# Performance work log

Measured on AMD Instinct MI355X. Metric: run time of the kernel, lower is better.

The kernel has to match this reference:

```python
import jax, jax.numpy as jnp
import numpy as np

EMBED_DIM = 768
NUM_HEADS = 12
HEAD_DIM = EMBED_DIM // NUM_HEADS
SCALE = HEAD_DIM ** -0.5
B, N = 8, 1024


def setup_inputs() -> dict:
    key = jax.random.key(0)
    ks = jax.random.split(key, 5)
    return {
        "x": jax.random.normal(ks[0], (B, N, EMBED_DIM), dtype=jnp.float32),
        "qkv_w": jax.random.normal(ks[1], (3 * EMBED_DIM, EMBED_DIM), dtype=jnp.float32) * 0.02,
        "qkv_b": jax.random.normal(ks[2], (3 * EMBED_DIM,), dtype=jnp.float32) * 0.02,
        "proj_w": jax.random.normal(ks[3], (EMBED_DIM, EMBED_DIM), dtype=jnp.float32) * 0.02,
        "proj_b": jax.random.normal(ks[4], (EMBED_DIM,), dtype=jnp.float32) * 0.02,
    }


def reference(x, qkv_w, qkv_b, proj_w, proj_b):
    b, n, c = x.shape
    h, hd = NUM_HEADS, HEAD_DIM
    # QKV projection: [b,n,3c]
    qkv = jnp.einsum("bnc,dc->bnd", x, qkv_w) + qkv_b
    qkv = qkv.reshape(b, n, 3, h, hd).transpose(2, 0, 3, 1, 4)  # [3,b,h,n,hd]
    q, k, v = qkv[0], qkv[1], qkv[2]
    # scaled dot-product attention (eager path; dropout is identity in eval)
    attn = jnp.einsum("bhqd,bhkd->bhqk", q, k) * SCALE
    attn = jax.nn.softmax(attn, axis=-1)
    out = jnp.einsum("bhqk,bhkd->bhqd", attn, v)  # [b,h,n,hd]
    out = out.transpose(0, 2, 1, 3).reshape(b, n, c)
    # output projection
    return jnp.einsum("bnc,dc->bnd", out, proj_w) + proj_b
```

## Files before the change

kernel.cpp:

```cpp
#include <hip/hip_runtime.h>
#include <hip/hip_bf16.h>

typedef __attribute__((ext_vector_type(4))) float f32x4;
typedef __attribute__((ext_vector_type(8))) short short8;
typedef unsigned short u16;

#define MFMA(a, b, c) __builtin_amdgcn_mfma_f32_16x16x32_bf16((a), (b), (c), 0, 0, 0)

#define WAITVM_BAR(N) do {                                          \
    asm volatile("s_waitcnt vmcnt(" #N ")" ::: "memory");           \
    __builtin_amdgcn_s_barrier();                                   \
    __builtin_amdgcn_sched_barrier(0);                              \
} while (0)
#define BAR2() do {                                                 \
    __builtin_amdgcn_sched_barrier(0);                              \
    __builtin_amdgcn_s_barrier();                                   \
    __builtin_amdgcn_sched_barrier(0);                              \
} while (0)

static constexpr int EMBED = 768;
static constexpr int NH = 12;
static constexpr int HD = 64;
static constexpr int BATCH = 8;
static constexpr int SEQ = 1024;

__device__ __forceinline__ u16 f2bu(float f) {
    __hip_bfloat16 h = __float2bfloat16(f);
    u16 u; __builtin_memcpy(&u, &h, 2); return u;
}
__device__ __forceinline__ float exp2a(float x) {
    float r; asm("v_exp_f32 %0, %1" : "=v"(r) : "v"(x)); return r;
}
__device__ __forceinline__ unsigned cvt_pk_bf16(float lo, float hi) {
    unsigned r; asm("v_cvt_pk_bf16_f32 %0, %1, %2" : "=v"(r) : "v"(lo), "v"(hi)); return r;
}
__device__ __forceinline__ float max3f(float a, float b, float c) {
    return fmaxf(fmaxf(a, b), c);
}

__global__ void cvt_bf16_k(const float* __restrict__ in, u16* __restrict__ out, int n) {
    int i = (blockIdx.x * blockDim.x + threadIdx.x) * 4;
    if (i >= n) return;
    float4 v = *reinterpret_cast<const float4*>(in + i);
    ushort4 o;
    o.x = f2bu(v.x); o.y = f2bu(v.y); o.z = f2bu(v.z); o.w = f2bu(v.w);
    *reinterpret_cast<ushort4*>(out + i) = o;
}

template <int EPI>
__global__ __launch_bounds__(256)
void gemm_bt_k(const u16* __restrict__ A, const u16* __restrict__ Bw,
               const float* __restrict__ bias,
               u16* __restrict__ q_out, u16* __restrict__ k_out,
               u16* __restrict__ vt_out, float* __restrict__ f_out)
{
    __shared__ __attribute__((aligned(16))) char smem[65536];
    const int tid  = threadIdx.x;
    const int wave = tid >> 6, lane = tid & 63;
    const int hi   = lane >> 4, l15 = lane & 15;
    const int wr   = wave >> 1, wc = wave & 1;
    const int bm   = blockIdx.x, bn = blockIdx.y;

    f32x4 acc[4][4] = {};

    const size_t arow0 = (size_t)bm * 128;
    const size_t brow0 = (size_t)bn * 128;

    auto stage = [&](int buf, int kt) {
        char* Ab = smem + buf * 32768;
        char* Bb = Ab + 16384;
#pragma unroll
        for (int c = 0; c < 4; ++c) {
            int ck   = c * 4 + wave;
            int p    = ck * 1024 + lane * 16;
            int row  = p >> 7;
            int pcol = (p & 127) ^ ((row & 7) << 4);
            const u16* srcA = A  + (arow0 + row) * EMBED + kt + (pcol >> 1);
            const u16* srcB = Bw + (brow0 + row) * EMBED + kt + (pcol >> 1);
            __builtin_amdgcn_global_load_lds((const __attribute__((address_space(1))) void*)srcA,
                                             (__attribute__((address_space(3))) void*)(Ab + ck * 1024), 16, 0, 0);
            __builtin_amdgcn_global_load_lds((const __attribute__((address_space(1))) void*)srcB,
                                             (__attribute__((address_space(3))) void*)(Bb + ck * 1024), 16, 0, 0);
        }
    };

    auto comp = [&](const char* Ab, const char* Bb) {
#pragma unroll
        for (int kk = 0; kk < 2; ++kk) {
            short8 af[4], bf[4];
#pragma unroll
            for (int mi = 0; mi < 4; ++mi) {
                int R  = wr * 64 + mi * 16 + l15;
                int Cb = kk * 64 + hi * 16;
                af[mi] = *reinterpret_cast<const short8*>(Ab + R * 128 + (Cb ^ ((R & 7) << 4)));
            }
#pragma unroll
            for (int ni = 0; ni < 4; ++ni) {
                int R  = wc * 64 + ni * 16 + l15;
                int Cb = kk * 64 + hi * 16;
                bf[ni] = *reinterpret_cast<const short8*>(Bb + R * 128 + (Cb ^ ((R & 7) << 4)));
            }
#pragma unroll
            for (int mi = 0; mi < 4; ++mi)
#pragma unroll
                for (int ni = 0; ni < 4; ++ni)
                    acc[mi][ni] = MFMA(af[mi], bf[ni], acc[mi][ni]);
        }
    };

    const char* A0 = smem;
    const char* B0 = smem + 16384;
    const char* A1 = smem + 32768;
    const char* B1 = smem + 49152;

    stage(0, 0);
#pragma unroll
    for (int tt = 0; tt < 5; ++tt) {
        stage(1, (2 * tt + 1) * 64);
        WAITVM_BAR(8);
        comp(A0, B0);
        BAR2();
        stage(0, (2 * tt + 2) * 64);
        WAITVM_BAR(8);
        comp(A1, B1);
        BAR2();
    }
    stage(1, 11 * 64);
    WAITVM_BAR(8);
    comp(A0, B0);
    BAR2();
    WAITVM_BAR(0);
    comp(A1, B1);

#pragma unroll
    for (int mi = 0; mi < 4; ++mi) {
        int crow0 = bm * 128 + wr * 64 + mi * 16 + hi * 4;
#pragma unroll
        for (int ni = 0; ni < 4; ++ni) {
            int ccol = bn * 128 + wc * 64 + ni * 16 + l15;
            float bv = bias[ccol];
            if constexpr (EPI == 0) {
                int which = ccol / 768;
                int rem   = ccol - which * 768;
                int hh = rem >> 6, hd = rem & 63;
                int bb = crow0 >> 10, nn0 = crow0 & 1023;
                size_t bh = (size_t)(bb * NH + hh);
                if (which == 2) {
                    uint2 pk;
                    pk.x = cvt_pk_bf16(acc[mi][ni][0] + bv, acc[mi][ni][1] + bv);
                    pk.y = cvt_pk_bf16(acc[mi][ni][2] + bv, acc[mi][ni][3] + bv);
                    *reinterpret_cast<uint2*>(&vt_out[(bh * HD + hd) * SEQ + nn0]) = pk;
                } else if (which == 0) {
#pragma unroll
                    for (int r = 0; r < 4; ++r)
                        q_out[(bh * SEQ + nn0 + r) * HD + hd] =
                            f2bu((acc[mi][ni][r] + bv) * 0.18033688f);
                } else {
#pragma unroll
                    for (int r = 0; r < 4; ++r)
                        k_out[(bh * SEQ + nn0 + r) * HD + hd] = f2bu(acc[mi][ni][r] + bv);
                }
            } else {
#pragma unroll
                for (int r = 0; r < 4; ++r)
                    f_out[(size_t)(crow0 + r) * EMBED + ccol] = acc[mi][ni][r] + bv;
            }
        }
    }
}

__global__ __launch_bounds__(256)
void attn_k(const u16* __restrict__ Q, const u16* __restrict__ K,
            const u16* __restrict__ Vt, u16* __restrict__ AO)
{
    __shared__ __attribute__((aligned(16))) u16 kls[2][4096];
    __shared__ __attribute__((aligned(16))) u16 vls[2][4096];
    __shared__ __attribute__((aligned(16))) u16 plds[4][32][72];

    const int tid = threadIdx.x;
    const int w   = tid >> 6, lane = tid & 63;
    const int hi  = lane >> 4, l15 = lane & 15;
    const int f   = blockIdx.x;
    const int xcd = f & 7, i = f >> 3;
    const int bh  = xcd * 12 + (i % 12);
    const int q0w = (i / 12) * 128 + w * 32;

    const u16* Qh = Q  + (size_t)bh * SEQ * HD;
    const u16* Kh = K  + (size_t)bh * SEQ * HD;
    const u16* Vh = Vt + (size_t)bh * HD * SEQ;

    auto stage = [&](int buf, int kt) {
#pragma unroll
        for (int c = 0; c < 4; ++c) {
            int ch   = c * 4 + w;
            int mc   = ch & 7;
            int p    = mc * 1024 + lane * 16;
            int row  = p >> 7;
            int colb = (p & 127) ^ ((row & 7) << 4);
            const u16* src;
            u16* dst;
            if (ch < 8) { src = Kh + (size_t)(kt + row) * HD + (colb >> 1); dst = kls[buf] + mc * 512; }
            else        { src = Vh + (size_t)row * SEQ + kt + (colb >> 1);  dst = vls[buf] + mc * 512; }
            __builtin_amdgcn_global_load_lds((const __attribute__((address_space(1))) void*)src,
                                             (__attribute__((address_space(3))) void*)dst, 16, 0, 0);
        }
    };

    stage(0, 0);

    short8 qf[2][2];
#pragma unroll
    for (int qh = 0; qh < 2; ++qh)
#pragma unroll
        for (int dh = 0; dh < 2; ++dh)
            qf[qh][dh] = *reinterpret_cast<const short8*>(
                Qh + (size_t)(q0w + qh * 16 + l15) * HD + dh * 32 + hi * 8);

    f32x4 accO[4][2] = {};
    float m0 = -1e30f, m1 = -1e30f, lp0 = 0.f, lp1 = 0.f;

    auto tile = [&](const u16* Kb, const u16* Vb) {
        f32x4 st[4][2] = {};
#pragma unroll
        for (int kb = 0; kb < 4; ++kb) {
            int R  = kb * 16 + l15;
            int sw = (R & 7) << 4;
            short8 kf0 = *reinterpret_cast<const short8*>(Kb + R * 64 + (((hi * 16) ^ sw) >> 1));
            short8 kf1 = *reinterpret_cast<const short8*>(Kb + R * 64 + (((64 + hi * 16) ^ sw) >> 1));
            st[kb][0] = MFMA(kf0, qf[0][0], st[kb][0]);
            st[kb][0] = MFMA(kf1, qf[0][1], st[kb][0]);
            st[kb][1] = MFMA(kf0, qf[1][0], st[kb][1]);
            st[kb][1] = MFMA(kf1, qf[1][1], st[kb][1]);
        }

        float p0 = max3f(st[0][0][0], st[0][0][1], st[0][0][2]);
        float p1 = max3f(st[0][0][3], st[1][0][0], st[1][0][1]);
        float p2 = max3f(st[1][0][2], st[1][0][3], st[2][0][0]);
        float p3 = max3f(st[2][0][1], st[2][0][2], st[2][0][3]);
        float p4 = max3f(st[3][0][0], st[3][0][1], st[3][0][2]);
        float tm0 = max3f(max3f(p0, p1, p2), max3f(p3, p4, st[3][0][3]), -1e30f);
        float r0 = max3f(st[0][1][0], st[0][1][1], st[0][1][2]);
        float r1 = max3f(st[0][1][3], st[1][1][0], st[1][1][1]);
        float r2 = max3f(st[1][1][2], st[1][1][3], st[2][1][0]);
        float r3 = max3f(st[2][1][1], st[2][1][2], st[2][1][3]);
        float r4 = max3f(st[3][1][0], st[3][1][1], st[3][1][2]);
        float tm1 = max3f(max3f(r0, r1, r2), max3f(r3, r4, st[3][1][3]), -1e30f);
        tm0 = fmaxf(tm0, __shfl_xor(tm0, 16, 64));
        tm0 = fmaxf(tm0, __shfl_xor(tm0, 32, 64));
        tm1 = fmaxf(tm1, __shfl_xor(tm1, 16, 64));
        tm1 = fmaxf(tm1, __shfl_xor(tm1, 32, 64));
        if (!__all((tm0 <= m0 + 8.f) && (tm1 <= m1 + 8.f))) {
            float mn0 = fmaxf(m0, tm0), mn1 = fmaxf(m1, tm1);
            float sc0 = exp2a(m0 - mn0), sc1 = exp2a(m1 - mn1);
            m0 = mn0; m1 = mn1;
            lp0 *= sc0; lp1 *= sc1;
#pragma unroll
            for (int db = 0; db < 4; ++db)
#pragma unroll
                for (int r = 0; r < 4; ++r) {
                    accO[db][0][r] *= sc0;
                    accO[db][1][r] *= sc1;
                }
        }

#pragma unroll
        for (int kb = 0; kb < 4; ++kb) {
            float e0 = exp2a(st[kb][0][0] - m0);
            float e1 = exp2a(st[kb][0][1] - m0);
            float e2 = exp2a(st[kb][0][2] - m0);
            float e3 = exp2a(st[kb][0][3] - m0);
            lp0 += (e0 + e1) + (e2 + e3);
            unsigned* d0 = reinterpret_cast<unsigned*>(&plds[w][l15][kb * 16 + hi * 4]);
            d0[0] = cvt_pk_bf16(e0, e1);
            d0[1] = cvt_pk_bf16(e2, e3);
            float g0 = exp2a(st[kb][1][0] - m1);
            float g1 = exp2a(st[kb][1][1] - m1);
            float g2 = exp2a(st[kb][1][2] - m1);
            float g3 = exp2a(st[kb][1][3] - m1);
            lp1 += (g0 + g1) + (g2 + g3);
            unsigned* d1 = reinterpret_cast<unsigned*>(&plds[w][16 + l15][kb * 16 + hi * 4]);
            d1[0] = cvt_pk_bf16(g0, g1);
            d1[1] = cvt_pk_bf16(g2, g3);
        }

        short8 pa[2][2];
#pragma unroll
        for (int qh = 0; qh < 2; ++qh)
#pragma unroll
            for (int kk = 0; kk < 2; ++kk)
                pa[qh][kk] = *reinterpret_cast<const short8*>(&plds[w][qh * 16 + l15][kk * 32 + hi * 8]);
        __builtin_amdgcn_sched_barrier(0);

#pragma unroll
        for (int db = 0; db < 4; ++db) {
            int R  = db * 16 + l15;
            int sw = (R & 7) << 4;
            short8 vf0 = *reinterpret_cast<const short8*>(Vb + R * 64 + (((hi * 16) ^ sw) >> 1));
            short8 vf1 = *reinterpret_cast<const short8*>(Vb + R * 64 + (((64 + hi * 16) ^ sw) >> 1));
            accO[db][0] = MFMA(vf0, pa[0][0], accO[db][0]);
            accO[db][0] = MFMA(vf1, pa[0][1], accO[db][0]);
            accO[db][1] = MFMA(vf0, pa[1][0], accO[db][1]);
            accO[db][1] = MFMA(vf1, pa[1][1], accO[db][1]);
        }
    };

    for (int tt = 0; tt < 7; ++tt) {
        stage(1, (2 * tt + 1) * 64);
        WAITVM_BAR(4);
        tile(kls[0], vls[0]);
        BAR2();
        stage(0, (2 * tt + 2) * 64);
        WAITVM_BAR(4);
        tile(kls[1], vls[1]);
        BAR2();
    }
    stage(1, 15 * 64);
    WAITVM_BAR(4);
    tile(kls[0], vls[0]);
    BAR2();
    WAITVM_BAR(0);
    tile(kls[1], vls[1]);

    lp0 += __shfl_xor(lp0, 16, 64);
    lp0 += __shfl_xor(lp0, 32, 64);
    lp1 += __shfl_xor(lp1, 16, 64);
    lp1 += __shfl_xor(lp1, 32, 64);
    float linv0 = 1.f / lp0, linv1 = 1.f / lp1;
    const int bb = bh / NH, hh = bh - bb * NH;
#pragma unroll
    for (int qh = 0; qh < 2; ++qh) {
        float linv = qh ? linv1 : linv0;
        size_t rowb = ((size_t)bb * SEQ + q0w + qh * 16 + l15) * EMBED + hh * HD;
#pragma unroll
        for (int db = 0; db < 4; ++db) {
            float o0 = accO[db][qh][0] * linv, o1 = accO[db][qh][1] * linv;
            float o2 = accO[db][qh][2] * linv, o3 = accO[db][qh][3] * linv;
            uint2 pkd;
            pkd.x = cvt_pk_bf16(o0, o1);
            pkd.y = cvt_pk_bf16(o2, o3);
            *reinterpret_cast<uint2*>(&AO[rowb + db * 16 + hi * 4]) = pkd;
        }
    }
}

extern "C" void kernel_launch(void* const* d_in, const int* in_sizes, int n_in,
                              void* d_out, int out_size, void* d_ws, size_t ws_size,
                              hipStream_t stream)
{
    const float* x      = (const float*)d_in[0];
    const float* qkv_w  = (const float*)d_in[1];
    const float* qkv_b  = (const float*)d_in[2];
    const float* proj_w = (const float*)d_in[3];
    const float* proj_b = (const float*)d_in[4];
    float* out = (float*)d_out;

    char* ws = (char*)d_ws;
    u16* xb  = (u16*)(ws);
    u16* wb  = (u16*)(ws + 12582912);
    u16* pw  = (u16*)(ws + 16121856);
    u16* qb  = (u16*)(ws + 17301504);
    u16* kb  = (u16*)(ws + 29884416);
    u16* vt  = (u16*)(ws + 42467328);
    u16* ao  = (u16*)(ws + 55050240);

    cvt_bf16_k<<<6144, 256, 0, stream>>>(x,      xb, BATCH * SEQ * EMBED);
    cvt_bf16_k<<<1728, 256, 0, stream>>>(qkv_w,  wb, 3 * EMBED * EMBED);
    cvt_bf16_k<<<576,  256, 0, stream>>>(proj_w, pw, EMBED * EMBED);

    gemm_bt_k<0><<<dim3(64, 18), 256, 0, stream>>>(xb, wb, qkv_b, qb, kb, vt, nullptr);
    attn_k<<<768, 256, 0, stream>>>(qb, kb, vt, ao);
    gemm_bt_k<1><<<dim3(64, 6), 256, 0, stream>>>(ao, pw, proj_b, nullptr, nullptr, nullptr, out);
}
```

Baseline: 114.0 us.

## Use 8 waves of 16 query rows in attention and permute P in registers

The attention kernel now runs 512 threads per block, with each wave owning 16 query rows instead of 32. This halves per-wave registers and raises occupancy, and each wave now stages one K chunk and one V chunk. The P matrix is no longer round-tripped through LDS; it is rearranged into MFMA operand layout with v_permlane32/16_swap, which removes that LDS store, load and scratch buffer. s_setprio is set around the MFMA sections. In exchange, K and V fragments are reread from LDS by twice as many waves, and the lane permutation must match the MFMA layout exactly.

New measurement: 107.1 us. 6.1% less time.

```diff
diff --git a/kernel.cpp b/kernel.cpp
--- a/kernel.cpp
+++ b/kernel.cpp
@@ -36,6 +36,17 @@
 }
 __device__ __forceinline__ float max3f(float a, float b, float c) {
     return fmaxf(fmaxf(a, b), c);
+}
+__device__ __forceinline__ void swap32(unsigned& a, unsigned& b) {
+    asm volatile("v_permlane32_swap_b32 %0, %1" : "+v"(a), "+v"(b));
+}
+__device__ __forceinline__ void swap16(unsigned& a, unsigned& b) {
+    asm volatile("v_permlane16_swap_b32 %0, %1" : "+v"(a), "+v"(b));
+}
+__device__ __forceinline__ short8 mk8(unsigned w0, unsigned w1, unsigned w2, unsigned w3) {
+    union { unsigned u[4]; short8 s; } c;
+    c.u[0] = w0; c.u[1] = w1; c.u[2] = w2; c.u[3] = w3;
+    return c.s;
 }
 
 __global__ void cvt_bf16_k(const float* __restrict__ in, u16* __restrict__ out, int n) {
@@ -169,13 +180,12 @@
     }
 }
 
-__global__ __launch_bounds__(256)
+__global__ __launch_bounds__(512, 6)
 void attn_k(const u16* __restrict__ Q, const u16* __restrict__ K,
             const u16* __restrict__ Vt, u16* __restrict__ AO)
 {
     __shared__ __attribute__((aligned(16))) u16 kls[2][4096];
     __shared__ __attribute__((aligned(16))) u16 vls[2][4096];
-    __shared__ __attribute__((aligned(16))) u16 plds[4][32][72];
 
     const int tid = threadIdx.x;
     const int w   = tid >> 6, lane = tid & 63;
@@ -183,163 +193,137 @@
     const int f   = blockIdx.x;
     const int xcd = f & 7, i = f >> 3;
     const int bh  = xcd * 12 + (i % 12);
-    const int q0w = (i / 12) * 128 + w * 32;
+    const int q0w = (i / 12) * 128 + w * 16;
 
     const u16* Qh = Q  + (size_t)bh * SEQ * HD;
     const u16* Kh = K  + (size_t)bh * SEQ * HD;
     const u16* Vh = Vt + (size_t)bh * HD * SEQ;
 
-    auto stage = [&](int buf, int kt) {
-#pragma unroll
-        for (int c = 0; c < 4; ++c) {
-            int ch   = c * 4 + w;
-            int mc   = ch & 7;
-            int p    = mc * 1024 + lane * 16;
-            int row  = p >> 7;
-            int colb = (p & 127) ^ ((row & 7) << 4);
-            const u16* src;
-            u16* dst;
-            if (ch < 8) { src = Kh + (size_t)(kt + row) * HD + (colb >> 1); dst = kls[buf] + mc * 512; }
-            else        { src = Vh + (size_t)row * SEQ + kt + (colb >> 1);  dst = vls[buf] + mc * 512; }
-            __builtin_amdgcn_global_load_lds((const __attribute__((address_space(1))) void*)src,
-                                             (__attribute__((address_space(3))) void*)dst, 16, 0, 0);
-        }
+    const int sp    = w * 1024 + lane * 16;
+    const int srow  = sp >> 7;
+    const int scolb = (sp & 127) ^ ((srow & 7) << 4);
+    const u16* kbase = Kh + (size_t)srow * HD + (scolb >> 1);
+    const u16* vbase = Vh + (size_t)srow * SEQ + (scolb >> 1);
+
+    auto stage = [&](int buf, int t) {
+        __builtin_amdgcn_global_load_lds(
+            (const __attribute__((address_space(1))) void*)(kbase + (size_t)t * 64 * HD),
+            (__attribute__((address_space(3))) void*)(&kls[buf][w * 512]), 16, 0, 0);
+        __builtin_amdgcn_global_load_lds(
+            (const __attribute__((address_space(1))) void*)(vbase + (size_t)t * 64),
+            (__attribute__((address_space(3))) void*)(&vls[buf][w * 512]), 16, 0, 0);
     };
 
     stage(0, 0);
 
-    short8 qf[2][2];
-#pragma unroll
-    for (int qh = 0; qh < 2; ++qh)
-#pragma unroll
-        for (int dh = 0; dh < 2; ++dh)
-            qf[qh][dh] = *reinterpret_cast<const short8*>(
-                Qh + (size_t)(q0w + qh * 16 + l15) * HD + dh * 32 + hi * 8);
-
-    f32x4 accO[4][2] = {};
-    float m0 = -1e30f, m1 = -1e30f, lp0 = 0.f, lp1 = 0.f;
+    short8 qf[2];
+#pragma unroll
+    for (int dh = 0; dh < 2; ++dh)
+        qf[dh] = *reinterpret_cast<const short8*>(
+            Qh + (size_t)(q0w + l15) * HD + dh * 32 + hi * 8);
+
+    f32x4 accO[4] = {};
+    float m = -1e30f, lp = 0.f;
 
     auto tile = [&](const u16* Kb, const u16* Vb) {
-        f32x4 st[4][2] = {};
+        f32x4 st[4] = {};
+        __builtin_amdgcn_s_setprio(1);
 #pragma unroll
         for (int kb = 0; kb < 4; ++kb) {
             int R  = kb * 16 + l15;
             int sw = (R & 7) << 4;
             short8 kf0 = *reinterpret_cast<const short8*>(Kb + R * 64 + (((hi * 16) ^ sw) >> 1));
             short8 kf1 = *reinterpret_cast<const short8*>(Kb + R * 64 + (((64 + hi * 16) ^ sw) >> 1));
-            st[kb][0] = MFMA(kf0, qf[0][0], st[kb][0]);
-            st[kb][0] = MFMA(kf1, qf[0][1], st[kb][0]);
-            st[kb][1] = MFMA(kf0, qf[1][0], st[kb][1]);
-            st[kb][1] = MFMA(kf1, qf[1][1], st[kb][1]);
-        }
-
-        float p0 = max3f(st[0][0][0], st[0][0][1], st[0][0][2]);
-        float p1 = max3f(st[0][0][3], st[1][0][0], st[1][0][1]);
-        float p2 = max3f(st[1][0][2], st[1][0][3], st[2][0][0]);
-        float p3 = max3f(st[2][0][1], st[2][0][2], st[2][0][3]);
-        float p4 = max3f(st[3][0][0], st[3][0][1], st[3][0][2]);
-        float tm0 = max3f(max3f(p0, p1, p2), max3f(p3, p4, st[3][0][3]), -1e30f);
-        float r0 = max3f(st[0][1][0], st[0][1][1], st[0][1][2]);
-        float r1 = max3f(st[0][1][3], st[1][1][0], st[1][1][1]);
-        float r2 = max3f(st[1][1][2], st[1][1][3], st[2][1][0]);
-        float r3 = max3f(st[2][1][1], st[2][1][2], st[2][1][3]);
-        float r4 = max3f(st[3][1][0], st[3][1][1], st[3][1][2]);
-        float tm1 = max3f(max3f(r0, r1, r2), max3f(r3, r4, st[3][1][3]), -1e30f);
-        tm0 = fmaxf(tm0, __shfl_xor(tm0, 16, 64));
-        tm0 = fmaxf(tm0, __shfl_xor(tm0, 32, 64));
-        tm1 = fmaxf(tm1, __shfl_xor(tm1, 16, 64));
-        tm1 = fmaxf(tm1, __shfl_xor(tm1, 32, 64));
-        if (!__all((tm0 <= m0 + 8.f) && (tm1 <= m1 + 8.f))) {
-            float mn0 = fmaxf(m0, tm0), mn1 = fmaxf(m1, tm1);
-            float sc0 = exp2a(m0 - mn0), sc1 = exp2a(m1 - mn1);
-            m0 = mn0; m1 = mn1;
-            lp0 *= sc0; lp1 *= sc1;
+            st[kb] = MFMA(kf0, qf[0], st[kb]);
+            st[kb] = MFMA(kf1, qf[1], st[kb]);
+        }
+        __builtin_amdgcn_s_setprio(0);
+
+        float t0 = max3f(st[0][0], st[0][1], st[0][2]);
+        float t1 = max3f(st[0][3], st[1][0], st[1][1]);
+        float t2 = max3f(st[1][2], st[1][3], st[2][0]);
+        float t3 = max3f(st[2][1], st[2][2], st[2][3]);
+        float t4 = max3f(st[3][0], st[3][1], st[3][2]);
+        float tm = fmaxf(max3f(t0, t1, t2), max3f(t3, t4, st[3][3]));
+        tm = fmaxf(tm, __shfl_xor(tm, 16, 64));
+        tm = fmaxf(tm, __shfl_xor(tm, 32, 64));
+        if (!__all(tm <= m + 8.f)) {
+            float mn = fmaxf(m, tm);
+            float sc = exp2a(m - mn);
+            m = mn;
+            lp *= sc;
 #pragma unroll
             for (int db = 0; db < 4; ++db)
 #pragma unroll
-                for (int r = 0; r < 4; ++r) {
-                    accO[db][0][r] *= sc0;
-                    accO[db][1][r] *= sc1;
-                }
-        }
-
+                for (int r = 0; r < 4; ++r) accO[db][r] *= sc;
+        }
+
+        unsigned X[4][2];
 #pragma unroll
         for (int kb = 0; kb < 4; ++kb) {
-            float e0 = exp2a(st[kb][0][0] - m0);
-            float e1 = exp2a(st[kb][0][1] - m0);
-            float e2 = exp2a(st[kb][0][2] - m0);
-            float e3 = exp2a(st[kb][0][3] - m0);
-            lp0 += (e0 + e1) + (e2 + e3);
-            unsigned* d0 = reinterpret_cast<unsigned*>(&plds[w][l15][kb * 16 + hi * 4]);
-            d0[0] = cvt_pk_bf16(e0, e1);
-            d0[1] = cvt_pk_bf16(e2, e3);
-            float g0 = exp2a(st[kb][1][0] - m1);
-            float g1 = exp2a(st[kb][1][1] - m1);
-            float g2 = exp2a(st[kb][1][2] - m1);
-            float g3 = exp2a(st[kb][1][3] - m1);
-            lp1 += (g0 + g1) + (g2 + g3);
-            unsigned* d1 = reinterpret_cast<unsigned*>(&plds[w][16 + l15][kb * 16 + hi * 4]);
-            d1[0] = cvt_pk_bf16(g0, g1);
-            d1[1] = cvt_pk_bf16(g2, g3);
-        }
-
-        short8 pa[2][2];
-#pragma unroll
-        for (int qh = 0; qh < 2; ++qh)
-#pragma unroll
-            for (int kk = 0; kk < 2; ++kk)
-                pa[qh][kk] = *reinterpret_cast<const short8*>(&plds[w][qh * 16 + l15][kk * 32 + hi * 8]);
-        __builtin_amdgcn_sched_barrier(0);
-
+            float e0 = exp2a(st[kb][0] - m);
+            float e1 = exp2a(st[kb][1] - m);
+            float e2 = exp2a(st[kb][2] - m);
+            float e3 = exp2a(st[kb][3] - m);
+            lp += (e0 + e1) + (e2 + e3);
+            X[kb][0] = cvt_pk_bf16(e0, e1);
+            X[kb][1] = cvt_pk_bf16(e2, e3);
+        }
+
+        unsigned a0 = X[0][0], b0 = X[1][0];
+        swap32(a0, b0); swap16(a0, b0);
+        unsigned a1 = X[0][1], b1 = X[1][1];
+        swap32(a1, b1); swap16(a1, b1);
+        unsigned a2 = X[2][0], b2 = X[3][0];
+        swap32(a2, b2); swap16(a2, b2);
+        unsigned a3 = X[2][1], b3 = X[3][1];
+        swap32(a3, b3); swap16(a3, b3);
+        short8 pa0 = mk8(a0, a1, b0, b1);
+        short8 pa1 = mk8(a2, a3, b2, b3);
+
+        __builtin_amdgcn_s_setprio(1);
 #pragma unroll
         for (int db = 0; db < 4; ++db) {
             int R  = db * 16 + l15;
             int sw = (R & 7) << 4;
             short8 vf0 = *reinterpret_cast<const short8*>(Vb + R * 64 + (((hi * 16) ^ sw) >> 1));
             short8 vf1 = *reinterpret_cast<const short8*>(Vb + R * 64 + (((64 + hi * 16) ^ sw) >> 1));
-            accO[db][0] = MFMA(vf0, pa[0][0], accO[db][0]);
-            accO[db][0] = MFMA(vf1, pa[0][1], accO[db][0]);
-            accO[db][1] = MFMA(vf0, pa[1][0], accO[db][1]);
-            accO[db][1] = MFMA(vf1, pa[1][1], accO[db][1]);
-        }
+            accO[db] = MFMA(vf0, pa0, accO[db]);
+            accO[db] = MFMA(vf1, pa1, accO[db]);
+        }
+        __builtin_amdgcn_s_setprio(0);
     };
 
     for (int tt = 0; tt < 7; ++tt) {
-        stage(1, (2 * tt + 1) * 64);
-        WAITVM_BAR(4);
+        stage(1, 2 * tt + 1);
+        WAITVM_BAR(2);
         tile(kls[0], vls[0]);
         BAR2();
-        stage(0, (2 * tt + 2) * 64);
-        WAITVM_BAR(4);
+        stage(0, 2 * tt + 2);
+        WAITVM_BAR(2);
         tile(kls[1], vls[1]);
         BAR2();
     }
-    stage(1, 15 * 64);
-    WAITVM_BAR(4);
+    stage(1, 15);
+    WAITVM_BAR(2);
     tile(kls[0], vls[0]);
     BAR2();
     WAITVM_BAR(0);
     tile(kls[1], vls[1]);
 
-    lp0 += __shfl_xor(lp0, 16, 64);
-    lp0 += __shfl_xor(lp0, 32, 64);
-    lp1 += __shfl_xor(lp1, 16, 64);
-    lp1 += __shfl_xor(lp1, 32, 64);
-    float linv0 = 1.f / lp0, linv1 = 1.f / lp1;
+    lp += __shfl_xor(lp, 16, 64);
+    lp += __shfl_xor(lp, 32, 64);
+    float linv = 1.f / lp;
     const int bb = bh / NH, hh = bh - bb * NH;
-#pragma unroll
-    for (int qh = 0; qh < 2; ++qh) {
-        float linv = qh ? linv1 : linv0;
-        size_t rowb = ((size_t)bb * SEQ + q0w + qh * 16 + l15) * EMBED + hh * HD;
-#pragma unroll
-        for (int db = 0; db < 4; ++db) {
-            float o0 = accO[db][qh][0] * linv, o1 = accO[db][qh][1] * linv;
-            float o2 = accO[db][qh][2] * linv, o3 = accO[db][qh][3] * linv;
-            uint2 pkd;
-            pkd.x = cvt_pk_bf16(o0, o1);
-            pkd.y = cvt_pk_bf16(o2, o3);
-            *reinterpret_cast<uint2*>(&AO[rowb + db * 16 + hi * 4]) = pkd;
-        }
+    size_t rowb = ((size_t)bb * SEQ + q0w + l15) * EMBED + hh * HD;
+#pragma unroll
+    for (int db = 0; db < 4; ++db) {
+        float o0 = accO[db][0] * linv, o1 = accO[db][1] * linv;
+        float o2 = accO[db][2] * linv, o3 = accO[db][3] * linv;
+        uint2 pkd;
+        pkd.x = cvt_pk_bf16(o0, o1);
+        pkd.y = cvt_pk_bf16(o2, o3);
+        *reinterpret_cast<uint2*>(&AO[rowb + db * 16 + hi * 4]) = pkd;
     }
 }
 
@@ -368,6 +352,6 @@
     cvt_bf16_k<<<576,  256, 0, stream>>>(proj_w, pw, EMBED * EMBED);
 
     gemm_bt_k<0><<<dim3(64, 18), 256, 0, stream>>>(xb, wb, qkv_b, qb, kb, vt, nullptr);
-    attn_k<<<768, 256, 0, stream>>>(qb, kb, vt, ao);
+    attn_k<<<768, 512, 0, stream>>>(qb, kb, vt, ao);
     gemm_bt_k<1><<<dim3(64, 6), 256, 0, stream>>>(ao, pw, proj_b, nullptr, nullptr, nullptr, out);
 }
```
